# Kernel optimization log

Measured on AMD Instinct MI355X. Metric: run time of the kernel, lower is better.

Reference implementation:

```python
import jax, jax.numpy as jnp
import numpy as np

H, W = 800, 800          # map height/width (Encoder init args)
B, N, SD = 1, 100000, 32 # batch, entity_num, scatter_dim
C = 8                    # number of spatial grids
SPATIAL = (120, 120)     # SPATIAL_SIZE


def setup_inputs() -> dict:
    key = jax.random.key(0)
    ks = jax.random.split(key, 8)
    return {
        "spatial": jax.random.normal(ks[0], (C, H, W), jnp.float32) * 200.0,
        "project_embeddings": jax.random.normal(ks[1], (B, N, SD), jnp.float32),
        "locations": jax.random.randint(ks[2], (B, N, 2), 0, 800, jnp.int64 if jax.config.jax_enable_x64 else jnp.int32),
        "scalar": jax.random.normal(ks[3], (B, 8), jnp.float32),
        "w1": jax.random.normal(ks[4], (8, 32), jnp.float32) * 0.35,
        "b1": jnp.zeros((32,), jnp.float32),
        "w2": jax.random.normal(ks[5], (32, 4), jnp.float32) * 0.25,
        "b2": jnp.zeros((4,), jnp.float32),
    }


def _scatter_connection(project_embeddings, locations):
    # project_embeddings: [B, N, SD], locations: [B, N, 2] (x, y) ints
    loc = locations.reshape(-1, 2)
    x = jnp.clip(loc[:, 0], 0, W - 1)
    y = jnp.clip(loc[:, 1], 0, H - 1)
    bias = jnp.repeat(jnp.arange(B, dtype=x.dtype), N) * (H * W)
    idx = y * W + x + bias                       # [B*N] flat indices into B*H*W
    src = project_embeddings.reshape(-1, SD).T   # [SD, B*N]
    smap = jnp.zeros((SD, B * H * W), project_embeddings.dtype)
    smap = smap.at[:, idx].add(src)              # duplicate-safe scatter_add
    smap = smap.reshape(SD, B, H, W).transpose(1, 0, 2, 3)  # [B, SD, H, W]
    return jax.image.resize(smap, (B, SD) + SPATIAL, method="bilinear")


def _process_grids(spatial):
    # crop is the full map (grid of ones -> all rows/cols kept)
    arr = jnp.nan_to_num(spatial, posinf=0.0)
    arr = jnp.where(arr > 255.0, 255.0, arr) / 255.0
    arr = jnp.rot90(arr, k=1, axes=(1, 2))       # torch rot90 default: CCW in last-2 dims
    arr = jax.image.resize(arr, (C,) + SPATIAL, method="bilinear")
    return arr.astype(jnp.float32)[None]         # [1, C, 120, 120]


def reference(spatial, project_embeddings, locations, scalar, w1, b1, w2, b2):
    scatter_entity = _scatter_connection(project_embeddings, locations)  # [B,32,120,120]
    processed_spatial = _process_grids(spatial)                          # [1, C,120,120]
    final_spatial = jnp.concatenate([processed_spatial, scatter_entity], axis=1)
    scalar_embeddings = jax.nn.relu(scalar @ w1 + b1)
    scalar_embeddings = jax.nn.relu(scalar_embeddings @ w2 + b2)
    return final_spatial, scalar_embeddings
```

## Files before the change

kernel.cpp:

```cpp
#include <hip/hip_runtime.h>
#include <hip/hip_bf16.h>
#include <math.h>

#define HMAP 800
#define WMAP 800
#define OHW  120
#define NCELL (OHW * OHW)
#define NCH  8
#define NPTS 100000
#define SDIM 32
#define CAP  32
#define NBIN1 121
#define NBINS (NBIN1 * NBIN1)

__device__ __forceinline__ float rscale() { return 800.0f / 120.0f; }

__device__ __forceinline__ float clipval(float v) {
    if (isnan(v)) v = 0.f;
    else if (isinf(v)) v = (v > 0.f) ? 0.f : -3.4028234663852886e38f;
    if (v > 255.f) v = 255.f;
    return v;
}

__device__ __forceinline__ float norm_sum(int i) {
    const float r = rscale();
    float c = ((float)i + 0.5f) * r - 0.5f;
    int j0 = (int)ceilf(c - r);
    float s = 0.f;
#pragma unroll
    for (int k = 0; k < 14; ++k) {
        int j = j0 + k;
        if (j < 0 || j >= HMAP) continue;
        s += fmaxf(0.f, 1.f - fabsf(c - (float)j) / r);
    }
    return s;
}

#define WS_COUNTS   0
#define WS_SPILLCUR 14641
#define WS_INVS     14656
#define WS_ENTRIES  14784
#define WS_SPILL    (WS_ENTRIES + NBINS * CAP * 2)
#define WS_T        (WS_SPILL + NPTS * 2)
#define WS_END      (WS_T + NCH * WMAP * OHW)
#define WS_REQ_BYTES ((size_t)WS_END * 4)

#define ZERO_BLOCKS 58
#define FILL_BLOCKS ((NPTS + 127) / 128)
#define RY_BLOCKS   (NCH * WMAP)
#define GA_BLOCKS   (NCELL / 4)
#define RX_BLOCKS   (NCH * OHW / 2)

__global__ void k_zero(int* __restrict__ counts, float* __restrict__ invS) {
    int gid = blockIdx.x * 256 + threadIdx.x;
    if (gid < 14656) counts[gid] = 0;
    if (gid < OHW) invS[gid] = 1.0f / norm_sum(gid);
}

__global__ void k_phase1(const float* __restrict__ spatial, const int* __restrict__ loc,
                         float* __restrict__ T, int* __restrict__ counts,
                         int2* __restrict__ entries, int2* __restrict__ spill,
                         int* __restrict__ spill_cur, const float* __restrict__ invS) {
    __shared__ float row[HMAP];
    if (blockIdx.x < FILL_BLOCKS) {
        int n = blockIdx.x * 128 + threadIdx.x;
        if (n >= NPTS) return;
        int2 xy = ((const int2*)loc)[n];
        int x = min(max(xy.x, 0), WMAP - 1);
        int y = min(max(xy.y, 0), HMAP - 1);
        const float r = rscale();
        int iy0 = (int)floorf(((float)y + 0.5f) / r - 0.5f);
        int ix0 = (int)floorf(((float)x + 0.5f) / r - 0.5f);
        int bin = (iy0 + 1) * NBIN1 + (ix0 + 1);
        int pos = (y << 10) | x;
        int slot = atomicAdd(&counts[bin], 1);
        if (slot < CAP) {
            entries[(size_t)bin * CAP + slot] = make_int2(n, pos);
        } else {
            int s = atomicAdd(spill_cur, 1);
            if (s < NPTS) spill[s] = make_int2((bin << 17) | n, pos);
        }
        return;
    }
    int bx = blockIdx.x - FILL_BLOCKS;
    int c = bx / WMAP, xx = bx % WMAP;
    const float* rp = spatial + (size_t)c * (HMAP * WMAP) + (size_t)xx * WMAP;
    for (int j = threadIdx.x; j < HMAP; j += 128) row[j] = clipval(rp[j]);
    __syncthreads();
    int oy = threadIdx.x;
    if (oy >= OHW) return;
    const float r = rscale();
    const float invR = 1.0f / r;
    float cy = ((float)oy + 0.5f) * r - 0.5f;
    int y0 = (int)ceilf(cy - r);
    float acc = 0.f;
#pragma unroll
    for (int k = 0; k < 14; ++k) {
        int j = y0 + k;
        float w = fmaxf(0.f, fmaf(-fabsf(cy - (float)j), invR, 1.f));
        w = (j >= 0 && j < HMAP) ? w : 0.f;
        int jc = min(max(j, 0), HMAP - 1);
        acc = fmaf(w, row[HMAP - 1 - jc], acc);
    }
    T[((size_t)c * WMAP + xx) * OHW + oy] = acc * (1.0f / 255.0f) * invS[oy];
}

__global__ void k_phase2(const float* __restrict__ T, const float* __restrict__ emb,
                         const int* __restrict__ counts, const int2* __restrict__ entries,
                         const int2* __restrict__ spill, const int* __restrict__ spill_cur,
                         const float* __restrict__ invS, float* __restrict__ out,
                         const float* __restrict__ scalar, const float* __restrict__ w1,
                         const float* __restrict__ b1, const float* __restrict__ w2,
                         const float* __restrict__ b2) {
    __shared__ int2 st[4][4][CAP];
    __shared__ float sh[32];
    int bid = blockIdx.x;
    if (bid < GA_BLOCKS) {
        int t = threadIdx.x;
        int wv = t >> 6;
        int cell = bid * 4 + wv;
        int lane = t & 63;
        int g = lane >> 4;
        int c2 = lane & 15;
        int iy = cell / OHW, ix = cell % OHW;
        const float r = rscale();
        const float invR = 1.0f / r;
        float cy = ((float)iy + 0.5f) * r - 0.5f;
        float cx = ((float)ix + 0.5f) * r - 0.5f;
        float invS2 = invS[iy] * invS[ix];
        int b00 = iy * NBIN1 + ix;

        int mybin = b00 + (g >> 1) * NBIN1 + (g & 1);
        int craw = counts[mybin];
        bool ovfany = __any(craw > CAP);
        int cnt = min(craw, CAP);
        int cmax = cnt;
        cmax = max(cmax, __shfl_xor(cmax, 16));
        cmax = max(cmax, __shfl_xor(cmax, 32));

#pragma unroll
        for (int ch = 0; ch < 2; ++ch) {
            int binrow = b00 + ch * NBIN1;
            const int2* base = entries + (size_t)binrow * CAP;
            int2 e = base[lane];
            int gs = ch * 2 + (lane >> 5);
            int slot = lane & 31;
            int scnt = min(counts[binrow + (lane >> 5)], CAP);
            int idx = 0;
            float w = 0.f;
            if (slot < scnt) {
                float py = (float)((e.y >> 10) & 1023);
                float px = (float)(e.y & 1023);
                float wy = fmaxf(0.f, fmaf(-fabsf(cy - py), invR, 1.f));
                float wx = fmaxf(0.f, fmaf(-fabsf(cx - px), invR, 1.f));
                w = wy * wx * invS2;
                idx = e.x;
            }
            st[wv][gs][slot] = make_int2(idx, __float_as_int(w));
        }

        const float2* embp = (const float2*)emb;
        float ax = 0.f, ay = 0.f;
        for (int i = 0; i < cmax; i += 4) {
            int2 s0 = st[wv][g][i + 0];
            int2 s1 = st[wv][g][i + 1];
            int2 s2 = st[wv][g][i + 2];
            int2 s3 = st[wv][g][i + 3];
            float2 v0 = embp[(size_t)s0.x * (SDIM / 2) + c2];
            float2 v1 = embp[(size_t)s1.x * (SDIM / 2) + c2];
            float2 v2 = embp[(size_t)s2.x * (SDIM / 2) + c2];
            float2 v3 = embp[(size_t)s3.x * (SDIM / 2) + c2];
            float w0 = __int_as_float(s0.y), w1_ = __int_as_float(s1.y);
            float w2_ = __int_as_float(s2.y), w3 = __int_as_float(s3.y);
            ax = fmaf(w0, v0.x, ax); ay = fmaf(w0, v0.y, ay);
            ax = fmaf(w1_, v1.x, ax); ay = fmaf(w1_, v1.y, ay);
            ax = fmaf(w2_, v2.x, ax); ay = fmaf(w2_, v2.y, ay);
            ax = fmaf(w3, v3.x, ax); ay = fmaf(w3, v3.y, ay);
        }

        if (ovfany) {
            int sn = min(spill_cur[0], NPTS);
            for (int s = 0; s < sn; ++s) {
                int2 e = spill[s];
                if ((e.x >> 17) == mybin) {
                    int n = e.x & 0x1FFFF;
                    float py = (float)((e.y >> 10) & 1023);
                    float px = (float)(e.y & 1023);
                    float wy = fmaxf(0.f, fmaf(-fabsf(cy - py), invR, 1.f));
                    float wx = fmaxf(0.f, fmaf(-fabsf(cx - px), invR, 1.f));
                    float w = wy * wx * invS2;
                    float2 v = embp[(size_t)n * (SDIM / 2) + c2];
                    ax = fmaf(w, v.x, ax); ay = fmaf(w, v.y, ay);
                }
            }
        }

        ax += __shfl_xor(ax, 16); ay += __shfl_xor(ay, 16);
        ax += __shfl_xor(ax, 32); ay += __shfl_xor(ay, 32);
        if (lane < 16) {
            out[(size_t)(NCH + 2 * c2) * NCELL + cell] = ax;
            out[(size_t)(NCH + 2 * c2 + 1) * NCELL + cell] = ay;
        }
        return;
    }
    if (bid < GA_BLOCKS + RX_BLOCKS) {
        int col = (bid - GA_BLOCKS) * 2 + (threadIdx.x >> 7);
        int oy = threadIdx.x & 127;
        if (oy >= OHW) return;
        int c = col / OHW, ox = col % OHW;
        const float r = rscale();
        const float invR = 1.0f / r;
        float cx = ((float)ox + 0.5f) * r - 0.5f;
        int x0 = (int)ceilf(cx - r);
        float acc = 0.f;
#pragma unroll
        for (int k = 0; k < 14; ++k) {
            int j = x0 + k;
            float w = fmaxf(0.f, fmaf(-fabsf(cx - (float)j), invR, 1.f));
            w = (j >= 0 && j < WMAP) ? w : 0.f;
            int jc = min(max(j, 0), WMAP - 1);
            acc = fmaf(w, T[((size_t)c * WMAP + jc) * OHW + oy], acc);
        }
        out[((size_t)c * OHW + oy) * OHW + ox] = acc * invS[ox];
        return;
    }
    int j = threadIdx.x;
    if (j < 32) {
        float a = b1[j];
        for (int i = 0; i < 8; ++i) a = fmaf(scalar[i], w1[i * 32 + j], a);
        sh[j] = fmaxf(a, 0.f);
    }
    __syncthreads();
    if (j < 4) {
        float a = b2[j];
        for (int i = 0; i < 32; ++i) a = fmaf(sh[i], w2[i * 4 + j], a);
        out[(size_t)(NCH + SDIM) * NCELL + j] = fmaxf(a, 0.f);
    }
}

__global__ void k_norm_fb(float* __restrict__ S) {
    int i = blockIdx.x * blockDim.x + threadIdx.x;
    if (i < OHW) S[i] = norm_sum(i);
}

__global__ void k_spatial_fb(const float* __restrict__ spatial, const float* __restrict__ S,
                             float* __restrict__ out) {
    int t = blockIdx.x * blockDim.x + threadIdx.x;
    if (t >= NCH * NCELL) return;
    int c = t / NCELL, rem = t % NCELL;
    int oy = rem / OHW, ox = rem % OHW;
    const float r = rscale();
    float cy = ((float)oy + 0.5f) * r - 0.5f;
    float cx = ((float)ox + 0.5f) * r - 0.5f;
    int y0 = (int)ceilf(cy - r);
    int x0 = (int)ceilf(cx - r);
    const float* sp = spatial + (size_t)c * (HMAP * WMAP);
    float acc = 0.f;
    for (int kx = 0; kx < 14; ++kx) {
        int col = x0 + kx;
        if (col < 0 || col >= WMAP) continue;
        float wxx = fmaxf(0.f, 1.f - fabsf(cx - (float)col) / r);
        if (wxx == 0.f) continue;
        const float* colp = sp + (size_t)col * WMAP;
        float accy = 0.f;
        for (int ky = 0; ky < 14; ++ky) {
            int j = y0 + ky;
            if (j < 0 || j >= HMAP) continue;
            float wyy = fmaxf(0.f, 1.f - fabsf(cy - (float)j) / r);
            accy = fmaf(wyy, clipval(colp[HMAP - 1 - j]), accy);
        }
        acc = fmaf(wxx, accy, acc);
    }
    out[t] = acc * (1.0f / 255.0f) / (S[oy] * S[ox]);
}

__global__ void k_scatter_fb(const float* __restrict__ emb, const int* __restrict__ loc,
                             const float* __restrict__ S, float* __restrict__ out) {
    int t = blockIdx.x * blockDim.x + threadIdx.x;
    if (t >= NPTS * SDIM) return;
    int n = t >> 5, c = t & 31;
    int x = min(max(loc[2 * n + 0], 0), WMAP - 1);
    int y = min(max(loc[2 * n + 1], 0), HMAP - 1);
    float e = emb[t];
    const float r = rscale();
    int iy0 = (int)floorf(((float)y + 0.5f) / r - 0.5f);
    int ix0 = (int)floorf(((float)x + 0.5f) / r - 0.5f);
    float* base = out + (size_t)(NCH + c) * NCELL;
#pragma unroll
    for (int a = 0; a < 2; ++a) {
        int iy = iy0 + a;
        if (iy < 0 || iy >= OHW) continue;
        float cyv = ((float)iy + 0.5f) * r - 0.5f;
        float wy = fmaxf(0.f, 1.f - fabsf(cyv - (float)y) / r) / S[iy];
#pragma unroll
        for (int b = 0; b < 2; ++b) {
            int ix = ix0 + b;
            if (ix < 0 || ix >= OHW) continue;
            float cxv = ((float)ix + 0.5f) * r - 0.5f;
            float wx = fmaxf(0.f, 1.f - fabsf(cxv - (float)x) / r) / S[ix];
            atomicAdd(base + iy * OHW + ix, e * wy * wx);
        }
    }
}

__global__ void k_mlp_fb(const float* __restrict__ scalar, const float* __restrict__ w1,
                         const float* __restrict__ b1, const float* __restrict__ w2,
                         const float* __restrict__ b2, float* __restrict__ out) {
    __shared__ float h[32];
    int j = threadIdx.x;
    if (j < 32) {
        float a = b1[j];
        for (int i = 0; i < 8; ++i) a = fmaf(scalar[i], w1[i * 32 + j], a);
        h[j] = fmaxf(a, 0.f);
    }
    __syncthreads();
    if (j < 4) {
        float a = b2[j];
        for (int i = 0; i < 32; ++i) a = fmaf(h[i], w2[i * 4 + j], a);
        out[(size_t)(NCH + SDIM) * NCELL + j] = fmaxf(a, 0.f);
    }
}

extern "C" void kernel_launch(void* const* d_in, const int* in_sizes, int n_in,
                              void* d_out, int out_size, void* d_ws, size_t ws_size,
                              hipStream_t stream) {
    const float* spatial = (const float*)d_in[0];
    const float* emb     = (const float*)d_in[1];
    const int*   loc     = (const int*)d_in[2];
    const float* scalar  = (const float*)d_in[3];
    const float* w1      = (const float*)d_in[4];
    const float* b1      = (const float*)d_in[5];
    const float* w2      = (const float*)d_in[6];
    const float* b2      = (const float*)d_in[7];
    float* out = (float*)d_out;

    int*   wsi = (int*)d_ws;
    float* wsf = (float*)d_ws;

    if (ws_size >= WS_REQ_BYTES) {
        int*   counts    = wsi + WS_COUNTS;
        int*   spill_cur = wsi + WS_SPILLCUR;
        float* invS      = wsf + WS_INVS;
        int2*  entries   = (int2*)(wsi + WS_ENTRIES);
        int2*  spill     = (int2*)(wsi + WS_SPILL);
        float* T         = wsf + WS_T;

        k_zero<<<ZERO_BLOCKS, 256, 0, stream>>>(counts, invS);
        k_phase1<<<FILL_BLOCKS + RY_BLOCKS, 128, 0, stream>>>(spatial, loc, T, counts,
                                                              entries, spill, spill_cur,
                                                              invS);
        k_phase2<<<GA_BLOCKS + RX_BLOCKS + 1, 256, 0, stream>>>(T, emb, counts, entries,
                                                                spill, spill_cur, invS,
                                                                out, scalar, w1, b1,
                                                                w2, b2);
    } else {
        float* S = wsf;
        hipMemsetAsync(d_out, 0, (size_t)out_size * sizeof(float), stream);
        k_norm_fb<<<1, 128, 0, stream>>>(S);
        k_spatial_fb<<<(NCH * NCELL + 255) / 256, 256, 0, stream>>>(spatial, S, out);
        k_scatter_fb<<<(NPTS * SDIM + 255) / 256, 256, 0, stream>>>(emb, loc, S, out);
        k_mlp_fb<<<1, 64, 0, stream>>>(scalar, w1, b1, w2, b2, out);
    }
}
```

Measured before the change: 38.10 us.

## Switch entity gather to per-bin scatter into partials plus combine kernel

The gather stage now processes each location bin once, with one wave per bin. Each 16-lane group computes the contribution to one of the four neighbouring output cells and writes it to a partial buffer P. A new combine kernel sums the four partials into the output. This replaces the per-cell approach that loaded four bins per cell, cutting redundant entry loads and embedding reads by roughly four times. The y-resize rows are now processed two per 256-thread block and normalize by the inline weight sum instead of the precomputed invS. In exchange the change adds an extra kernel launch and a 7 MB partial buffer round-trip.

```diff
diff --git a/kernel.cpp b/kernel.cpp
--- a/kernel.cpp
+++ b/kernel.cpp
@@ -42,14 +42,16 @@
 #define WS_ENTRIES  14784
 #define WS_SPILL    (WS_ENTRIES + NBINS * CAP * 2)
 #define WS_T        (WS_SPILL + NPTS * 2)
-#define WS_END      (WS_T + NCH * WMAP * OHW)
+#define WS_P        (WS_T + NCH * WMAP * OHW)
+#define WS_END      (WS_P + 4 * NCELL * SDIM)
 #define WS_REQ_BYTES ((size_t)WS_END * 4)
 
 #define ZERO_BLOCKS 58
-#define FILL_BLOCKS ((NPTS + 127) / 128)
-#define RY_BLOCKS   (NCH * WMAP)
-#define GA_BLOCKS   (NCELL / 4)
+#define FILL_BLOCKS ((NPTS + 255) / 256)
+#define RY_BLOCKS   (NCH * WMAP / 2)
+#define GB_BLOCKS   ((NBINS + 3) / 4)
 #define RX_BLOCKS   (NCH * OHW / 2)
+#define CB_BLOCKS   (NCELL / 16)
 
 __global__ void k_zero(int* __restrict__ counts, float* __restrict__ invS) {
     int gid = blockIdx.x * 256 + threadIdx.x;
@@ -60,10 +62,10 @@
 __global__ void k_phase1(const float* __restrict__ spatial, const int* __restrict__ loc,
                          float* __restrict__ T, int* __restrict__ counts,
                          int2* __restrict__ entries, int2* __restrict__ spill,
-                         int* __restrict__ spill_cur, const float* __restrict__ invS) {
-    __shared__ float row[HMAP];
+                         int* __restrict__ spill_cur) {
+    __shared__ float row[2][HMAP];
     if (blockIdx.x < FILL_BLOCKS) {
-        int n = blockIdx.x * 128 + threadIdx.x;
+        int n = blockIdx.x * 256 + threadIdx.x;
         if (n >= NPTS) return;
         int2 xy = ((const int2*)loc)[n];
         int x = min(max(xy.x, 0), WMAP - 1);
@@ -82,107 +84,84 @@
         }
         return;
     }
-    int bx = blockIdx.x - FILL_BLOCKS;
+    int bx = (blockIdx.x - FILL_BLOCKS) * 2 + (threadIdx.x >> 7);
+    int hw = threadIdx.x & 127;
     int c = bx / WMAP, xx = bx % WMAP;
+    int rsel = threadIdx.x >> 7;
     const float* rp = spatial + (size_t)c * (HMAP * WMAP) + (size_t)xx * WMAP;
-    for (int j = threadIdx.x; j < HMAP; j += 128) row[j] = clipval(rp[j]);
+    for (int j = hw; j < HMAP; j += 128) row[rsel][j] = clipval(rp[j]);
     __syncthreads();
-    int oy = threadIdx.x;
+    int oy = hw;
     if (oy >= OHW) return;
     const float r = rscale();
     const float invR = 1.0f / r;
     float cy = ((float)oy + 0.5f) * r - 0.5f;
     int y0 = (int)ceilf(cy - r);
-    float acc = 0.f;
+    float acc = 0.f, ws = 0.f;
 #pragma unroll
     for (int k = 0; k < 14; ++k) {
         int j = y0 + k;
         float w = fmaxf(0.f, fmaf(-fabsf(cy - (float)j), invR, 1.f));
         w = (j >= 0 && j < HMAP) ? w : 0.f;
         int jc = min(max(j, 0), HMAP - 1);
-        acc = fmaf(w, row[HMAP - 1 - jc], acc);
-    }
-    T[((size_t)c * WMAP + xx) * OHW + oy] = acc * (1.0f / 255.0f) * invS[oy];
+        ws += w;
+        acc = fmaf(w, row[rsel][HMAP - 1 - jc], acc);
+    }
+    T[((size_t)c * WMAP + xx) * OHW + oy] = acc / (255.f * ws);
 }
 
 __global__ void k_phase2(const float* __restrict__ T, const float* __restrict__ emb,
                          const int* __restrict__ counts, const int2* __restrict__ entries,
                          const int2* __restrict__ spill, const int* __restrict__ spill_cur,
-                         const float* __restrict__ invS, float* __restrict__ out,
+                         const float* __restrict__ invS, float* __restrict__ P,
+                         float* __restrict__ out,
                          const float* __restrict__ scalar, const float* __restrict__ w1,
                          const float* __restrict__ b1, const float* __restrict__ w2,
                          const float* __restrict__ b2) {
-    __shared__ int2 st[4][4][CAP];
+    __shared__ int2 st[4][CAP];
     __shared__ float sh[32];
     int bid = blockIdx.x;
-    if (bid < GA_BLOCKS) {
+    if (bid < GB_BLOCKS) {
         int t = threadIdx.x;
         int wv = t >> 6;
-        int cell = bid * 4 + wv;
+        int bin = bid * 4 + wv;
+        if (bin >= NBINS) return;
         int lane = t & 63;
-        int g = lane >> 4;
+        int q = lane >> 4;
         int c2 = lane & 15;
-        int iy = cell / OHW, ix = cell % OHW;
+        int by = bin / NBIN1, bx = bin % NBIN1;
+        int cell_y = by - 1 + (q >> 1);
+        int cell_x = bx - 1 + (q & 1);
+        bool valid = (cell_y >= 0 && cell_y < OHW && cell_x >= 0 && cell_x < OHW);
+        int cyi = min(max(cell_y, 0), OHW - 1), cxi = min(max(cell_x, 0), OHW - 1);
         const float r = rscale();
         const float invR = 1.0f / r;
-        float cy = ((float)iy + 0.5f) * r - 0.5f;
-        float cx = ((float)ix + 0.5f) * r - 0.5f;
-        float invS2 = invS[iy] * invS[ix];
-        int b00 = iy * NBIN1 + ix;
-
-        int mybin = b00 + (g >> 1) * NBIN1 + (g & 1);
-        int craw = counts[mybin];
-        bool ovfany = __any(craw > CAP);
+        float cy = ((float)cell_y + 0.5f) * r - 0.5f;
+        float cx = ((float)cell_x + 0.5f) * r - 0.5f;
+        float invS2 = valid ? (invS[cyi] * invS[cxi]) : 0.f;
+
+        int craw = counts[bin];
         int cnt = min(craw, CAP);
-        int cmax = cnt;
-        cmax = max(cmax, __shfl_xor(cmax, 16));
-        cmax = max(cmax, __shfl_xor(cmax, 32));
-
-#pragma unroll
-        for (int ch = 0; ch < 2; ++ch) {
-            int binrow = b00 + ch * NBIN1;
-            const int2* base = entries + (size_t)binrow * CAP;
-            int2 e = base[lane];
-            int gs = ch * 2 + (lane >> 5);
-            int slot = lane & 31;
-            int scnt = min(counts[binrow + (lane >> 5)], CAP);
-            int idx = 0;
-            float w = 0.f;
-            if (slot < scnt) {
-                float py = (float)((e.y >> 10) & 1023);
-                float px = (float)(e.y & 1023);
-                float wy = fmaxf(0.f, fmaf(-fabsf(cy - py), invR, 1.f));
-                float wx = fmaxf(0.f, fmaf(-fabsf(cx - px), invR, 1.f));
-                w = wy * wx * invS2;
-                idx = e.x;
-            }
-            st[wv][gs][slot] = make_int2(idx, __float_as_int(w));
-        }
+        if (lane < CAP) st[wv][lane] = entries[(size_t)bin * CAP + lane];
 
         const float2* embp = (const float2*)emb;
         float ax = 0.f, ay = 0.f;
-        for (int i = 0; i < cmax; i += 4) {
-            int2 s0 = st[wv][g][i + 0];
-            int2 s1 = st[wv][g][i + 1];
-            int2 s2 = st[wv][g][i + 2];
-            int2 s3 = st[wv][g][i + 3];
-            float2 v0 = embp[(size_t)s0.x * (SDIM / 2) + c2];
-            float2 v1 = embp[(size_t)s1.x * (SDIM / 2) + c2];
-            float2 v2 = embp[(size_t)s2.x * (SDIM / 2) + c2];
-            float2 v3 = embp[(size_t)s3.x * (SDIM / 2) + c2];
-            float w0 = __int_as_float(s0.y), w1_ = __int_as_float(s1.y);
-            float w2_ = __int_as_float(s2.y), w3 = __int_as_float(s3.y);
-            ax = fmaf(w0, v0.x, ax); ay = fmaf(w0, v0.y, ay);
-            ax = fmaf(w1_, v1.x, ax); ay = fmaf(w1_, v1.y, ay);
-            ax = fmaf(w2_, v2.x, ax); ay = fmaf(w2_, v2.y, ay);
-            ax = fmaf(w3, v3.x, ax); ay = fmaf(w3, v3.y, ay);
-        }
-
-        if (ovfany) {
+        for (int i = 0; i < cnt; ++i) {
+            int2 e = st[wv][i];
+            float py = (float)((e.y >> 10) & 1023);
+            float px = (float)(e.y & 1023);
+            float wy = fmaxf(0.f, fmaf(-fabsf(cy - py), invR, 1.f));
+            float wx = fmaxf(0.f, fmaf(-fabsf(cx - px), invR, 1.f));
+            float w = wy * wx * invS2;
+            float2 v = embp[(size_t)e.x * (SDIM / 2) + c2];
+            ax = fmaf(w, v.x, ax);
+            ay = fmaf(w, v.y, ay);
+        }
+        if (craw > CAP) {
             int sn = min(spill_cur[0], NPTS);
             for (int s = 0; s < sn; ++s) {
                 int2 e = spill[s];
-                if ((e.x >> 17) == mybin) {
+                if ((e.x >> 17) == bin) {
                     int n = e.x & 0x1FFFF;
                     float py = (float)((e.y >> 10) & 1023);
                     float px = (float)(e.y & 1023);
@@ -194,17 +173,15 @@
                 }
             }
         }
-
-        ax += __shfl_xor(ax, 16); ay += __shfl_xor(ay, 16);
-        ax += __shfl_xor(ax, 32); ay += __shfl_xor(ay, 32);
-        if (lane < 16) {
-            out[(size_t)(NCH + 2 * c2) * NCELL + cell] = ax;
-            out[(size_t)(NCH + 2 * c2 + 1) * NCELL + cell] = ay;
+        if (valid) {
+            float2* pp = (float2*)P;
+            pp[((size_t)q * NCELL + cell_y * OHW + cell_x) * (SDIM / 2) + c2] =
+                make_float2(ax, ay);
         }
         return;
     }
-    if (bid < GA_BLOCKS + RX_BLOCKS) {
-        int col = (bid - GA_BLOCKS) * 2 + (threadIdx.x >> 7);
+    if (bid < GB_BLOCKS + RX_BLOCKS) {
+        int col = (bid - GB_BLOCKS) * 2 + (threadIdx.x >> 7);
         int oy = threadIdx.x & 127;
         if (oy >= OHW) return;
         int c = col / OHW, ox = col % OHW;
@@ -236,6 +213,21 @@
         for (int i = 0; i < 32; ++i) a = fmaf(sh[i], w2[i * 4 + j], a);
         out[(size_t)(NCH + SDIM) * NCELL + j] = fmaxf(a, 0.f);
     }
+}
+
+__global__ void k_combine(const float* __restrict__ P, float* __restrict__ out) {
+    int t = threadIdx.x;
+    int cell = blockIdx.x * 16 + (t >> 4);
+    int c2 = t & 15;
+    const float2* pp = (const float2*)P;
+    float ax = 0.f, ay = 0.f;
+#pragma unroll
+    for (int q = 0; q < 4; ++q) {
+        float2 v = pp[((size_t)q * NCELL + cell) * (SDIM / 2) + c2];
+        ax += v.x; ay += v.y;
+    }
+    out[(size_t)(NCH + 2 * c2) * NCELL + cell] = ax;
+    out[(size_t)(NCH + 2 * c2 + 1) * NCELL + cell] = ay;
 }
 
 __global__ void k_norm_fb(float* __restrict__ S) {
@@ -344,15 +336,16 @@
         int2*  entries   = (int2*)(wsi + WS_ENTRIES);
         int2*  spill     = (int2*)(wsi + WS_SPILL);
         float* T         = wsf + WS_T;
+        float* P         = wsf + WS_P;
 
         k_zero<<<ZERO_BLOCKS, 256, 0, stream>>>(counts, invS);
-        k_phase1<<<FILL_BLOCKS + RY_BLOCKS, 128, 0, stream>>>(spatial, loc, T, counts,
-                                                              entries, spill, spill_cur,
-                                                              invS);
-        k_phase2<<<GA_BLOCKS + RX_BLOCKS + 1, 256, 0, stream>>>(T, emb, counts, entries,
+        k_phase1<<<FILL_BLOCKS + RY_BLOCKS, 256, 0, stream>>>(spatial, loc, T, counts,
+                                                              entries, spill, spill_cur);
+        k_phase2<<<GB_BLOCKS + RX_BLOCKS + 1, 256, 0, stream>>>(T, emb, counts, entries,
                                                                 spill, spill_cur, invS,
-                                                                out, scalar, w1, b1,
+                                                                P, out, scalar, w1, b1,
                                                                 w2, b2);
+        k_combine<<<CB_BLOCKS, 256, 0, stream>>>(P, out);
     } else {
         float* S = wsf;
         hipMemsetAsync(d_out, 0, (size_t)out_size * sizeof(float), stream);
```

Result: faster. 37.31 us (-2.1%).
